# Performance work log

Hardware: AMD Instinct MI355X
Metric: run time of the kernel (lower is better)

Reference implementation:

```python
import jax, jax.numpy as jnp
import numpy as np

D_MODEL = 512
N_HEADS = 8
D_K = D_MODEL // N_HEADS  # 64
EPS = 1e-5


def setup_inputs() -> dict:
    key = jax.random.key(0)
    ks = jax.random.split(key, 16)
    s = 0.02
    B, T = 4, 2048
    return {
        "x": jax.random.normal(ks[0], (B, T, D_MODEL), dtype=jnp.float32),
        # per-head q/k/v projections stacked over heads: [H, d_model, d_k]
        "Wq": jax.random.normal(ks[1], (N_HEADS, D_MODEL, D_K), dtype=jnp.float32) * s,
        "bq": jnp.zeros((N_HEADS, D_K), dtype=jnp.float32),
        "Wk": jax.random.normal(ks[2], (N_HEADS, D_MODEL, D_K), dtype=jnp.float32) * s,
        "bk": jnp.zeros((N_HEADS, D_K), dtype=jnp.float32),
        "Wv": jax.random.normal(ks[3], (N_HEADS, D_MODEL, D_K), dtype=jnp.float32) * s,
        "bv": jnp.zeros((N_HEADS, D_K), dtype=jnp.float32),
        "Wp": jax.random.normal(ks[4], (D_MODEL, D_MODEL), dtype=jnp.float32) * s,
        "bp": jnp.zeros((D_MODEL,), dtype=jnp.float32),
        "W1": jax.random.normal(ks[5], (D_MODEL, 4 * D_MODEL), dtype=jnp.float32) * s,
        "b1": jnp.zeros((4 * D_MODEL,), dtype=jnp.float32),
        "W2": jax.random.normal(ks[6], (4 * D_MODEL, D_MODEL), dtype=jnp.float32) * s,
        "b2": jnp.zeros((D_MODEL,), dtype=jnp.float32),
        "g1": jnp.ones((D_MODEL,), dtype=jnp.float32),
        "be1": jnp.zeros((D_MODEL,), dtype=jnp.float32),
        "g2": jnp.ones((D_MODEL,), dtype=jnp.float32),
        "be2": jnp.zeros((D_MODEL,), dtype=jnp.float32),
    }


def _layer_norm(x, g, b):
    mu = jnp.mean(x, axis=-1, keepdims=True)
    var = jnp.var(x, axis=-1, keepdims=True)
    return (x - mu) * jax.lax.rsqrt(var + EPS) * g + b


def _block(x, Wq, bq, Wk, bk, Wv, bv, Wp, bp, W1, b1, W2, b2, g1, be1, g2, be2):
    B, T, _ = x.shape
    h = _layer_norm(x, g1, be1)
    # batched per-head projections: [B, H, T, d_k]
    q = jnp.einsum('btd,hdk->bhtk', h, Wq) + bq[:, None, :]
    k = jnp.einsum('btd,hdk->bhtk', h, Wk) + bk[:, None, :]
    v = jnp.einsum('btd,hdk->bhtk', h, Wv) + bv[:, None, :]
    scores = jnp.einsum('bhtk,bhsk->bhts', q, k)  # [B, H, T, T]
    causal = jnp.tril(jnp.ones((T, T), dtype=bool))
    # faithful to source: mask with -1e9 BEFORE dividing by sqrt(d_k)
    scores = jnp.where(causal, scores, jnp.float32(-1e9))
    attn = jax.nn.softmax(scores / jnp.float32(np.sqrt(D_K)), axis=-1)
    o = jnp.einsum('bhts,bhsk->bhtk', attn, v)  # [B, H, T, d_k]
    o = o.transpose(0, 2, 1, 3).reshape(B, T, D_MODEL)  # concat heads
    x = x + o @ Wp + bp
    h2 = _layer_norm(x, g2, be2)
    ff = jax.nn.relu(h2 @ W1 + b1) @ W2 + b2
    return x + ff


def reference(x, Wq, bq, Wk, bk, Wv, bv, Wp, bp, W1, b1, W2, b2, g1, be1, g2, be2):
    return _block(x, Wq, bq, Wk, bk, Wv, bv, Wp, bp, W1, b1, W2, b2, g1, be1, g2, be2)
```

## Files before the change

kernel.cpp:

```cpp
#include <hip/hip_runtime.h>
#include <hip/hip_bf16.h>
#include <math.h>

#define BATCH 4
#define SEQ   2048
#define DM    512
#define NH    8
#define DK    64
#define FF    2048
#define BT    (BATCH * SEQ)

#define SCALE_Q 0.18033688011112042f

typedef short bf16x8 __attribute__((ext_vector_type(8)));
typedef float f32x4  __attribute__((ext_vector_type(4)));

static __device__ inline short f2bf(float f) {
  union { float f; unsigned u; } v; v.f = f;
  unsigned r = (v.u + 0x7fffu + ((v.u >> 16) & 1u)) >> 16;
  return (short)r;
}

static __device__ __forceinline__ void gload16(const short* g, short* l) {
  __builtin_amdgcn_global_load_lds(
      (const __attribute__((address_space(1))) void*)g,
      (__attribute__((address_space(3))) void*)l, 16, 0, 0);
}

static __device__ __forceinline__ void xcd_swizzle(int& bx, int& by) {
  int gx = gridDim.x;
  int nwg = gx * gridDim.y;
  int id = blockIdx.x + gx * blockIdx.y;
  int nid = (id & 7) * (nwg >> 3) + (id >> 3);
  bx = nid % gx;
  by = nid / gx;
}

__global__ __launch_bounds__(256) void ln_kernel(
    const float* __restrict__ x, const float* __restrict__ gamma,
    const float* __restrict__ beta, short* __restrict__ out) {
  int row = blockIdx.x;
  const float* xr = x + (size_t)row * DM;
  int t = threadIdx.x;
  float v0 = xr[t], v1 = xr[t + 256];
  float s = v0 + v1;
  float sq = v0 * v0 + v1 * v1;
  for (int off = 32; off; off >>= 1) {
    s  += __shfl_xor(s, off);
    sq += __shfl_xor(sq, off);
  }
  __shared__ float ssum[4], ssq[4];
  int wave = t >> 6, lane = t & 63;
  if (lane == 0) { ssum[wave] = s; ssq[wave] = sq; }
  __syncthreads();
  if (t == 0) {
    float S = ssum[0] + ssum[1] + ssum[2] + ssum[3];
    float Q = ssq[0] + ssq[1] + ssq[2] + ssq[3];
    float mu = S * (1.0f / DM);
    float var = Q * (1.0f / DM) - mu * mu;
    ssum[0] = mu;
    ssq[0] = rsqrtf(var + 1e-5f);
  }
  __syncthreads();
  float mu = ssum[0], rstd = ssq[0];
  short* orow = out + (size_t)row * DM;
  orow[t]       = f2bf((v0 - mu) * rstd * gamma[t]       + beta[t]);
  orow[t + 256] = f2bf((v1 - mu) * rstd * gamma[t + 256] + beta[t + 256]);
}

__global__ __launch_bounds__(256) void wconv_kernel(
    const float* Wq, const float* Wk, const float* Wv,
    const float* Wp, const float* W1, const float* W2,
    short* wqkv, short* wpt, short* w1t, short* w2t) {
  int z = blockIdx.z;
  const float* src; short* dst; int R, C;
  if (z < 24) {
    int m = z >> 3, hh = z & 7;
    const float* s0 = (m == 0) ? Wq : (m == 1) ? Wk : Wv;
    src = s0 + (size_t)hh * 512 * 64;
    dst = wqkv + ((size_t)(m * 512 + hh * 64)) * 512;
    R = 512; C = 64;
  } else if (z == 24) { src = Wp; dst = wpt; R = 512;  C = 512;  }
  else if (z == 25)   { src = W1; dst = w1t; R = 512;  C = 2048; }
  else                { src = W2; dst = w2t; R = 2048; C = 512;  }
  int tx = blockIdx.x, ty = blockIdx.y;
  if (tx >= C / 64 || ty >= R / 64) return;
  __shared__ float Ts[64][68];
  int t = threadIdx.x;
  int r = t >> 2, c0 = (t & 3) * 16;
  const float* sp = src + (size_t)(ty * 64 + r) * C + tx * 64 + c0;
#pragma unroll
  for (int i = 0; i < 16; i += 4) {
    float4 v = *(const float4*)(sp + i);
    Ts[c0 + i + 0][r] = v.x; Ts[c0 + i + 1][r] = v.y;
    Ts[c0 + i + 2][r] = v.z; Ts[c0 + i + 3][r] = v.w;
  }
  __syncthreads();
  short* dp = dst + (size_t)(tx * 64 + r) * R + ty * 64 + c0;
  short tmp[16];
#pragma unroll
  for (int i = 0; i < 16; ++i) tmp[i] = f2bf(Ts[r][c0 + i]);
  *(int4*)(dp)     = *(int4*)&tmp[0];
  *(int4*)(dp + 8) = *(int4*)&tmp[8];
}

template<int TM, int TN>
__device__ __forceinline__ void gemm_core(
    const short* __restrict__ A, const short* __restrict__ Bw,
    int m0, int n0, int K, short* smem, f32x4 (&acc)[TM / 32][TN / 32]) {
  constexpr int AF = TM / 32, BF = TN / 32;
  constexpr int AC = TM / 64, BC = TN / 64;
  constexpr int BUFS = (TM + TN) * 32;
  int t = threadIdx.x;
  int wave = t >> 6, lane = t & 63, quad = lane >> 4, l16 = lane & 15;
  int wr = wave >> 1, wc = wave & 1;

  size_t aoff[AC], boff[BC];
  int aldsoff[AC], bldsoff[BC];
#pragma unroll
  for (int c = 0; c < AC; ++c) {
    int p = c * 256 + t, row = p >> 2, lg = (p & 3) ^ ((row >> 1) & 3);
    aoff[c] = (size_t)(m0 + row) * K + lg * 8;
    aldsoff[c] = c * 2048 + wave * 512;
  }
#pragma unroll
  for (int c = 0; c < BC; ++c) {
    int p = c * 256 + t, row = p >> 2, lg = (p & 3) ^ ((row >> 1) & 3);
    boff[c] = (size_t)(n0 + row) * K + lg * 8;
    bldsoff[c] = TM * 32 + c * 2048 + wave * 512;
  }

#pragma unroll
  for (int c = 0; c < AC; ++c) gload16(A + aoff[c], smem + aldsoff[c]);
#pragma unroll
  for (int c = 0; c < BC; ++c) gload16(Bw + boff[c], smem + bldsoff[c]);

  int physo = (quad ^ ((l16 >> 1) & 3)) * 8;

  for (int k0 = 0; k0 < K; k0 += 32) {
    short* cbuf = smem + ((k0 >> 5) & 1) * BUFS;
    __syncthreads();
    if (k0 + 32 < K) {
      short* nbuf = smem + (((k0 >> 5) & 1) ^ 1) * BUFS;
#pragma unroll
      for (int c = 0; c < AC; ++c) gload16(A + aoff[c] + k0 + 32, nbuf + aldsoff[c]);
#pragma unroll
      for (int c = 0; c < BC; ++c) gload16(Bw + boff[c] + k0 + 32, nbuf + bldsoff[c]);
    }
    bf16x8 af[AF], bfr[BF];
#pragma unroll
    for (int i = 0; i < AF; ++i)
      af[i] = *(const bf16x8*)&cbuf[(wr * (TM / 2) + i * 16 + l16) * 32 + physo];
#pragma unroll
    for (int j = 0; j < BF; ++j)
      bfr[j] = *(const bf16x8*)&cbuf[TM * 32 + (wc * (TN / 2) + j * 16 + l16) * 32 + physo];
#pragma unroll
    for (int i = 0; i < AF; ++i)
#pragma unroll
      for (int j = 0; j < BF; ++j)
        acc[i][j] = __builtin_amdgcn_mfma_f32_16x16x32_bf16(bfr[j], af[i], acc[i][j], 0, 0, 0);
  }
}

template<int TM, int TN>
__global__ __launch_bounds__(256) void mgemm_kernel(
    const short* __restrict__ A, const short* __restrict__ Bw,
    const float* __restrict__ bias, const float* __restrict__ res,
    void* __restrict__ C, int N, int K, int dorelu, int bf16out) {
  __shared__ __align__(16) short smem[(TM + TN) * 64];
  f32x4 acc[TM / 32][TN / 32];
  f32x4 zf = {0.f, 0.f, 0.f, 0.f};
#pragma unroll
  for (int i = 0; i < TM / 32; ++i)
#pragma unroll
    for (int j = 0; j < TN / 32; ++j) acc[i][j] = zf;
  int bx, by;
  xcd_swizzle(bx, by);
  int m0 = by * TM, n0 = bx * TN;
  gemm_core<TM, TN>(A, Bw, m0, n0, K, smem, acc);

  int t = threadIdx.x;
  int wave = t >> 6, lane = t & 63, quad = lane >> 4, l16 = lane & 15;
  int wr = wave >> 1, wc = wave & 1;
#pragma unroll
  for (int i = 0; i < TM / 32; ++i) {
    int m = m0 + wr * (TM / 2) + i * 16 + l16;
#pragma unroll
    for (int j = 0; j < TN / 32; ++j) {
      int nb = n0 + wc * (TN / 2) + j * 16 + quad * 4;
      float4 bv = *(const float4*)&bias[nb];
      float v[4] = {acc[i][j][0] + bv.x, acc[i][j][1] + bv.y,
                    acc[i][j][2] + bv.z, acc[i][j][3] + bv.w};
      if (dorelu) {
#pragma unroll
        for (int r = 0; r < 4; ++r) v[r] = fmaxf(v[r], 0.0f);
      }
      size_t off = (size_t)m * N + nb;
      if (res) {
        float4 rv = *(const float4*)(res + off);
        v[0] += rv.x; v[1] += rv.y; v[2] += rv.z; v[3] += rv.w;
      }
      if (bf16out) {
        short tmp[4] = {f2bf(v[0]), f2bf(v[1]), f2bf(v[2]), f2bf(v[3])};
        *(int2*)((short*)C + off) = *(int2*)tmp;
      } else {
        float4 outv = {v[0], v[1], v[2], v[3]};
        *(float4*)((float*)C + off) = outv;
      }
    }
  }
}

__global__ __launch_bounds__(256) void qkv_kernel(
    const short* __restrict__ A, const short* __restrict__ Bw,
    const float* __restrict__ bq, const float* __restrict__ bk,
    const float* __restrict__ bv,
    short* __restrict__ q, short* __restrict__ k, short* __restrict__ vt) {
  __shared__ __align__(16) short smem[17408];
  f32x4 acc[4][4];
  f32x4 zf = {0.f, 0.f, 0.f, 0.f};
#pragma unroll
  for (int i = 0; i < 4; ++i)
#pragma unroll
    for (int j = 0; j < 4; ++j) acc[i][j] = zf;
  int bx, by;
  xcd_swizzle(bx, by);
  int m0 = by * 128, n0 = bx * 128;
  gemm_core<128, 128>(A, Bw, m0, n0, DM, smem, acc);

  int t = threadIdx.x;
  int wave = t >> 6, lane = t & 63, quad = lane >> 4, l16 = lane & 15;
  int wr = wave >> 1, wc = wave & 1;

  if (n0 < 1024) {
    short* out = (n0 < 512) ? q : k;
    const float* bias = (n0 < 512) ? bq + n0 : bk + (n0 - 512);
    float scale = (n0 < 512) ? SCALE_Q : 1.0f;
    int ncol0 = (n0 < 512) ? n0 : n0 - 512;
#pragma unroll
    for (int i = 0; i < 4; ++i) {
      int m = m0 + wr * 64 + i * 16 + l16;
#pragma unroll
      for (int j = 0; j < 4; ++j) {
        int nb = wc * 64 + j * 16 + quad * 4;
        float4 bvv = *(const float4*)&bias[nb];
        short tmp[4];
        tmp[0] = f2bf((acc[i][j][0] + bvv.x) * scale);
        tmp[1] = f2bf((acc[i][j][1] + bvv.y) * scale);
        tmp[2] = f2bf((acc[i][j][2] + bvv.z) * scale);
        tmp[3] = f2bf((acc[i][j][3] + bvv.w) * scale);
        *(int2*)(out + (size_t)m * DM + ncol0 + nb) = *(int2*)tmp;
      }
    }
  } else {
    const float* bias = bv + (n0 - 1024);
    __syncthreads();
    short* Ts = smem;
#pragma unroll
    for (int i = 0; i < 4; ++i) {
      int ml = wr * 64 + i * 16 + l16;
#pragma unroll
      for (int j = 0; j < 4; ++j) {
        int nb = wc * 64 + j * 16 + quad * 4;
        float4 bvv = *(const float4*)&bias[nb];
        Ts[(nb + 0) * 136 + ml] = f2bf(acc[i][j][0] + bvv.x);
        Ts[(nb + 1) * 136 + ml] = f2bf(acc[i][j][1] + bvv.y);
        Ts[(nb + 2) * 136 + ml] = f2bf(acc[i][j][2] + bvv.z);
        Ts[(nb + 3) * 136 + ml] = f2bf(acc[i][j][3] + bvv.w);
      }
    }
    __syncthreads();
    int nl = t >> 1, half = (t & 1) * 64;
    int gn = (n0 - 1024) + nl;
    int hh = gn >> 6, dk = gn & 63;
    int bidx = m0 >> 11, s0 = (m0 & 2047) + half;
    short* dst = vt + ((size_t)((bidx * NH + hh) * DK + dk)) * SEQ + s0;
    const short* srcT = &Ts[nl * 136 + half];
#pragma unroll
    for (int i2 = 0; i2 < 64; i2 += 8)
      *(int4*)(dst + i2) = *(const int4*)(srcT + i2);
  }
}

template<bool DIAG>
static __device__ __forceinline__ void attn_tile(
    const short* __restrict__ KsC, const short* __restrict__ VsC,
    short* __restrict__ Psw, const bf16x8& qf0, const bf16x8& qf1,
    f32x4 (&o_acc)[4], float& l_part, int quad, int l16,
    int keyb0, int qrow) {
  f32x4 zf = {0.f, 0.f, 0.f, 0.f};
  int sw = l16 & 7;

#pragma unroll
  for (int nt = 0; nt < 4; ++nt) {
    int krow = nt * 16 + l16;
    bf16x8 ka0 = *(const bf16x8*)&KsC[krow * 64 + ((quad ^ sw) * 8)];
    bf16x8 ka1 = *(const bf16x8*)&KsC[krow * 64 + (((4 + quad) ^ sw) * 8)];
    f32x4 s = __builtin_amdgcn_mfma_f32_16x16x32_bf16(ka0, qf0, zf, 0, 0, 0);
    s = __builtin_amdgcn_mfma_f32_16x16x32_bf16(ka1, qf1, s, 0, 0, 0);
    int keyb = keyb0 + nt * 16 + quad * 4;
    float pr[4];
#pragma unroll
    for (int r = 0; r < 4; ++r) {
      float e = exp2f(s[r]);
      pr[r] = (DIAG && (keyb + r > qrow)) ? 0.0f : e;
      l_part += pr[r];
    }
    unsigned pk0 = __builtin_amdgcn_perm(
        __float_as_uint(pr[1]), __float_as_uint(pr[0]), 0x07060302u);
    unsigned pk1 = __builtin_amdgcn_perm(
        __float_as_uint(pr[3]), __float_as_uint(pr[2]), 0x07060302u);
    int2 w = {(int)pk0, (int)pk1};
    *(int2*)&Psw[l16 * 64 + (((nt * 2 + (quad >> 1)) ^ sw) << 3) +
                 ((quad & 1) * 4)] = w;
  }

  bf16x8 apf0 = *(const bf16x8*)&Psw[l16 * 64 + ((quad ^ sw) * 8)];
  bf16x8 apf1 = *(const bf16x8*)&Psw[l16 * 64 + (((4 + quad) ^ sw) * 8)];
  __builtin_amdgcn_s_setprio(1);
#pragma unroll
  for (int nt2 = 0; nt2 < 4; ++nt2) {
    int vrow = nt2 * 16 + l16;
    bf16x8 vf0 = *(const bf16x8*)&VsC[vrow * 64 + ((quad ^ sw) * 8)];
    bf16x8 vf1 = *(const bf16x8*)&VsC[vrow * 64 + (((4 + quad) ^ sw) * 8)];
    o_acc[nt2] = __builtin_amdgcn_mfma_f32_16x16x32_bf16(vf0, apf0, o_acc[nt2], 0, 0, 0);
    o_acc[nt2] = __builtin_amdgcn_mfma_f32_16x16x32_bf16(vf1, apf1, o_acc[nt2], 0, 0, 0);
  }
  __builtin_amdgcn_s_setprio(0);
}

__global__ __launch_bounds__(256) void fattn_kernel(
    const short* __restrict__ Q, const short* __restrict__ Kg,
    const short* __restrict__ Vt, short* __restrict__ O) {
  int id = blockIdx.x + 32 * (blockIdx.y + NH * blockIdx.z);
  int c = id & 7, j = id >> 3;
  int g = c * 4 + (j & 3);
  int qt = 31 - (j >> 2);
  int h = g & 7, b = g >> 3;
  int q0 = qt * 64;
  int t = threadIdx.x, wave = t >> 6, lane = t & 63, quad = lane >> 4, l16 = lane & 15;

  __shared__ __align__(16) short Ks[2][64 * 64];
  __shared__ __align__(16) short Vs[2][64 * 64];
  __shared__ __align__(16) short Ps[4][16 * 64];

  f32x4 zf = {0.f, 0.f, 0.f, 0.f};
  const short* qp = Q + ((size_t)(b * SEQ + q0 + wave * 16 + l16)) * DM + h * DK;
  bf16x8 qf0 = *(const bf16x8*)(qp + quad * 8);
  bf16x8 qf1 = *(const bf16x8*)(qp + 32 + quad * 8);

  f32x4 o_acc[4];
  float l_part = 0.0f;
#pragma unroll
  for (int i = 0; i < 4; ++i) o_acc[i] = zf;

  const short* kb = Kg + ((size_t)(b * SEQ)) * DM + h * DK;
  const short* vb = Vt + ((size_t)((b * NH + h) * DK)) * SEQ;

  int row0 = t >> 3,         lg0 = (t & 7) ^ (row0 & 7);
  int row1 = (256 + t) >> 3, lg1 = ((256 + t) & 7) ^ (row1 & 7);
  const short* kp0 = kb + (size_t)row0 * DM + lg0 * 8;
  const short* kp1 = kb + (size_t)row1 * DM + lg1 * 8;
  const short* vp0 = vb + (size_t)row0 * SEQ + lg0 * 8;
  const short* vp1 = vb + (size_t)row1 * SEQ + lg1 * 8;
  int lo0 = wave * 512, lo1 = 2048 + wave * 512;

#define STAGE_KV(B) do {                                     \
    gload16(kp0, &Ks[B][lo0]); gload16(kp1, &Ks[B][lo1]);    \
    gload16(vp0, &Vs[B][lo0]); gload16(vp1, &Vs[B][lo1]);    \
    kp0 += 64 * DM; kp1 += 64 * DM; vp0 += 64; vp1 += 64; } while (0)

  STAGE_KV(0);

  int qrow = q0 + wave * 16 + l16;
  short* Psw = &Ps[wave][0];

  int buf = 0;
  for (int kt = 0; kt < qt; ++kt) {
    __syncthreads();
    STAGE_KV(buf ^ 1);
    attn_tile<false>(&Ks[buf][0], &Vs[buf][0], Psw, qf0, qf1,
                     o_acc, l_part, quad, l16, 0, qrow);
    buf ^= 1;
  }
  __syncthreads();
  attn_tile<true>(&Ks[buf][0], &Vs[buf][0], Psw, qf0, qf1,
                  o_acc, l_part, quad, l16, qt * 64, qrow);

  float lf = l_part;
  lf += __shfl_xor(lf, 16);
  lf += __shfl_xor(lf, 32);
  float inv = 1.0f / lf;
  short* orow = O + ((size_t)(b * SEQ) + qrow) * DM + h * DK;
#pragma unroll
  for (int nt2 = 0; nt2 < 4; ++nt2) {
    short tmp[4];
#pragma unroll
    for (int r = 0; r < 4; ++r) tmp[r] = f2bf(o_acc[nt2][r] * inv);
    *(int2*)(orow + nt2 * 16 + quad * 4) = *(int2*)tmp;
  }
#undef STAGE_KV
}

extern "C" void kernel_launch(void* const* d_in, const int* in_sizes, int n_in,
                              void* d_out, int out_size, void* d_ws, size_t ws_size,
                              hipStream_t stream) {
  const float* x   = (const float*)d_in[0];
  const float* Wq  = (const float*)d_in[1];
  const float* bq  = (const float*)d_in[2];
  const float* Wk  = (const float*)d_in[3];
  const float* bk  = (const float*)d_in[4];
  const float* Wv  = (const float*)d_in[5];
  const float* bv  = (const float*)d_in[6];
  const float* Wp  = (const float*)d_in[7];
  const float* bp  = (const float*)d_in[8];
  const float* W1  = (const float*)d_in[9];
  const float* b1  = (const float*)d_in[10];
  const float* W2  = (const float*)d_in[11];
  const float* b2  = (const float*)d_in[12];
  const float* g1  = (const float*)d_in[13];
  const float* be1 = (const float*)d_in[14];
  const float* g2  = (const float*)d_in[15];
  const float* be2 = (const float*)d_in[16];
  float* out = (float*)d_out;

  char* wsb = (char*)d_ws;
  const size_t SB = (size_t)BT * DM * 2;
  short* h    = (short*)(wsb);
  short* q    = (short*)(wsb + SB);
  short* k    = (short*)(wsb + 2 * SB);
  short* vt   = (short*)(wsb + 3 * SB);
  short* o    = (short*)(wsb + 4 * SB);
  float* x2   = (float*)(wsb + 5 * SB);
  short* h2   = (short*)(wsb + 5 * SB + (size_t)BT * DM * 4);
  short* ff   = (short*)(wsb + 6 * SB + (size_t)BT * DM * 4);
  short* wqkv = (short*)(wsb + 6 * SB + (size_t)BT * DM * 4 + (size_t)BT * FF * 2);
  short* wpt  = wqkv + 1536 * 512;
  short* w1t  = wpt + 512 * 512;
  short* w2t  = w1t + 2048 * 512;

  dim3 blk(256);

  wconv_kernel<<<dim3(32, 32, 27), blk, 0, stream>>>(Wq, Wk, Wv, Wp, W1, W2,
                                                     wqkv, wpt, w1t, w2t);
  ln_kernel<<<BT, blk, 0, stream>>>(x, g1, be1, h);

  qkv_kernel<<<dim3(12, 64), blk, 0, stream>>>(h, wqkv, bq, bk, bv, q, k, vt);

  fattn_kernel<<<dim3(32, NH, BATCH), blk, 0, stream>>>(q, k, vt, o);

  mgemm_kernel<128, 64><<<dim3(8, 64), blk, 0, stream>>>(o, wpt, bp, x, x2, DM, DM, 0, 0);
  ln_kernel<<<BT, blk, 0, stream>>>(x2, g2, be2, h2);
  mgemm_kernel<128, 128><<<dim3(16, 64), blk, 0, stream>>>(h2, w1t, b1, nullptr, ff, FF, DM, 1, 1);
  mgemm_kernel<128, 64><<<dim3(8, 64), blk, 0, stream>>>(ff, w2t, b2, x2, out, DM, FF, 0, 0);
}
```

Before: 273.4 us.

## Add 64x64-tile GEMM for N=512 projections and compact weight-conversion grid

Adds a dedicated 64x64 tiled bf16 MFMA GEMM kernel with double-buffered LDS loads and uses it for the output projection and the FFN down-projection. Launching 1024 blocks instead of 512 should fill the GPU's CUs better on these N=512 GEMMs. The trade-off is more per-tile load overhead and less reuse. Separately, the weight-conversion launch drops from a 32x32x27 grid, where most blocks exit immediately, to a flat 768-block grid with no idle blocks.

```diff
diff --git a/kernel.cpp b/kernel.cpp
--- a/kernel.cpp
+++ b/kernel.cpp
@@ -72,19 +72,25 @@
     const float* Wq, const float* Wk, const float* Wv,
     const float* Wp, const float* W1, const float* W2,
     short* wqkv, short* wpt, short* w1t, short* w2t) {
-  int z = blockIdx.z;
-  const float* src; short* dst; int R, C;
-  if (z < 24) {
+  int id = blockIdx.x;
+  const float* src; short* dst; int R, C, tx, ty;
+  if (id < 192) {
+    int z = id >> 3;
     int m = z >> 3, hh = z & 7;
     const float* s0 = (m == 0) ? Wq : (m == 1) ? Wk : Wv;
     src = s0 + (size_t)hh * 512 * 64;
     dst = wqkv + ((size_t)(m * 512 + hh * 64)) * 512;
-    R = 512; C = 64;
-  } else if (z == 24) { src = Wp; dst = wpt; R = 512;  C = 512;  }
-  else if (z == 25)   { src = W1; dst = w1t; R = 512;  C = 2048; }
-  else                { src = W2; dst = w2t; R = 2048; C = 512;  }
-  int tx = blockIdx.x, ty = blockIdx.y;
-  if (tx >= C / 64 || ty >= R / 64) return;
+    R = 512; C = 64; tx = 0; ty = id & 7;
+  } else if (id < 256) {
+    int w = id - 192; src = Wp; dst = wpt; R = 512; C = 512;
+    tx = w & 7; ty = w >> 3;
+  } else if (id < 512) {
+    int w = id - 256; src = W1; dst = w1t; R = 512; C = 2048;
+    tx = w & 31; ty = w >> 5;
+  } else {
+    int w = id - 512; src = W2; dst = w2t; R = 2048; C = 512;
+    tx = w & 7; ty = w >> 3;
+  }
   __shared__ float Ts[64][68];
   int t = threadIdx.x;
   int r = t >> 2, c0 = (t & 3) * 16;
@@ -188,6 +194,101 @@
 #pragma unroll
     for (int j = 0; j < TN / 32; ++j) {
       int nb = n0 + wc * (TN / 2) + j * 16 + quad * 4;
+      float4 bv = *(const float4*)&bias[nb];
+      float v[4] = {acc[i][j][0] + bv.x, acc[i][j][1] + bv.y,
+                    acc[i][j][2] + bv.z, acc[i][j][3] + bv.w};
+      if (dorelu) {
+#pragma unroll
+        for (int r = 0; r < 4; ++r) v[r] = fmaxf(v[r], 0.0f);
+      }
+      size_t off = (size_t)m * N + nb;
+      if (res) {
+        float4 rv = *(const float4*)(res + off);
+        v[0] += rv.x; v[1] += rv.y; v[2] += rv.z; v[3] += rv.w;
+      }
+      if (bf16out) {
+        short tmp[4] = {f2bf(v[0]), f2bf(v[1]), f2bf(v[2]), f2bf(v[3])};
+        *(int2*)((short*)C + off) = *(int2*)tmp;
+      } else {
+        float4 outv = {v[0], v[1], v[2], v[3]};
+        *(float4*)((float*)C + off) = outv;
+      }
+    }
+  }
+}
+
+__global__ __launch_bounds__(256) void mgemm64_kernel(
+    const short* __restrict__ A, const short* __restrict__ Bw,
+    const float* __restrict__ bias, const float* __restrict__ res,
+    void* __restrict__ C, int N, int K, int dorelu, int bf16out) {
+  __shared__ __align__(16) short smem[2 * 8192];
+  f32x4 acc[2][2];
+  f32x4 zf = {0.f, 0.f, 0.f, 0.f};
+#pragma unroll
+  for (int i = 0; i < 2; ++i)
+#pragma unroll
+    for (int j = 0; j < 2; ++j) acc[i][j] = zf;
+  int bx, by;
+  xcd_swizzle(bx, by);
+  int m0 = by * 64, n0 = bx * 64;
+
+  int t = threadIdx.x;
+  int wave = t >> 6, lane = t & 63, quad = lane >> 4, l16 = lane & 15;
+  int wr = wave >> 1, wc = wave & 1;
+
+  int rA0 = t >> 3,        lg0 = (t & 7) ^ (rA0 & 7);
+  int rA1 = 32 + (t >> 3), lg1 = (t & 7) ^ (rA1 & 7);
+  size_t aoff0 = (size_t)(m0 + rA0) * K + lg0 * 8;
+  size_t aoff1 = (size_t)(m0 + rA1) * K + lg1 * 8;
+  size_t boff0 = (size_t)(n0 + rA0) * K + lg0 * 8;
+  size_t boff1 = (size_t)(n0 + rA1) * K + lg1 * 8;
+  int lo0 = wave * 512, lo1 = 2048 + wave * 512;
+
+  gload16(A + aoff0, smem + lo0);
+  gload16(A + aoff1, smem + lo1);
+  gload16(Bw + boff0, smem + 4096 + lo0);
+  gload16(Bw + boff1, smem + 4096 + lo1);
+
+  int sw = l16 & 7;
+
+  for (int k0 = 0; k0 < K; k0 += 64) {
+    short* cbuf = smem + ((k0 >> 6) & 1) * 8192;
+    __syncthreads();
+    if (k0 + 64 < K) {
+      short* nbuf = smem + (((k0 >> 6) & 1) ^ 1) * 8192;
+      gload16(A + aoff0 + k0 + 64, nbuf + lo0);
+      gload16(A + aoff1 + k0 + 64, nbuf + lo1);
+      gload16(Bw + boff0 + k0 + 64, nbuf + 4096 + lo0);
+      gload16(Bw + boff1 + k0 + 64, nbuf + 4096 + lo1);
+    }
+    bf16x8 af0[2], af1[2], bf0[2], bf1[2];
+#pragma unroll
+    for (int i = 0; i < 2; ++i) {
+      int r = wr * 32 + i * 16 + l16;
+      af0[i] = *(const bf16x8*)&cbuf[r * 64 + ((quad ^ sw) * 8)];
+      af1[i] = *(const bf16x8*)&cbuf[r * 64 + (((4 + quad) ^ sw) * 8)];
+    }
+#pragma unroll
+    for (int j = 0; j < 2; ++j) {
+      int r = wc * 32 + j * 16 + l16;
+      bf0[j] = *(const bf16x8*)&cbuf[4096 + r * 64 + ((quad ^ sw) * 8)];
+      bf1[j] = *(const bf16x8*)&cbuf[4096 + r * 64 + (((4 + quad) ^ sw) * 8)];
+    }
+#pragma unroll
+    for (int i = 0; i < 2; ++i)
+#pragma unroll
+      for (int j = 0; j < 2; ++j) {
+        acc[i][j] = __builtin_amdgcn_mfma_f32_16x16x32_bf16(bf0[j], af0[i], acc[i][j], 0, 0, 0);
+        acc[i][j] = __builtin_amdgcn_mfma_f32_16x16x32_bf16(bf1[j], af1[i], acc[i][j], 0, 0, 0);
+      }
+  }
+
+#pragma unroll
+  for (int i = 0; i < 2; ++i) {
+    int m = m0 + wr * 32 + i * 16 + l16;
+#pragma unroll
+    for (int j = 0; j < 2; ++j) {
+      int nb = n0 + wc * 32 + j * 16 + quad * 4;
       float4 bv = *(const float4*)&bias[nb];
       float v[4] = {acc[i][j][0] + bv.x, acc[i][j][1] + bv.y,
                     acc[i][j][2] + bv.z, acc[i][j][3] + bv.w};
@@ -441,16 +542,16 @@
 
   dim3 blk(256);
 
-  wconv_kernel<<<dim3(32, 32, 27), blk, 0, stream>>>(Wq, Wk, Wv, Wp, W1, W2,
-                                                     wqkv, wpt, w1t, w2t);
+  wconv_kernel<<<dim3(768), blk, 0, stream>>>(Wq, Wk, Wv, Wp, W1, W2,
+                                              wqkv, wpt, w1t, w2t);
   ln_kernel<<<BT, blk, 0, stream>>>(x, g1, be1, h);
 
   qkv_kernel<<<dim3(12, 64), blk, 0, stream>>>(h, wqkv, bq, bk, bv, q, k, vt);
 
   fattn_kernel<<<dim3(32, NH, BATCH), blk, 0, stream>>>(q, k, vt, o);
 
-  mgemm_kernel<128, 64><<<dim3(8, 64), blk, 0, stream>>>(o, wpt, bp, x, x2, DM, DM, 0, 0);
+  mgemm64_kernel<<<dim3(8, 128), blk, 0, stream>>>(o, wpt, bp, x, x2, DM, DM, 0, 0);
   ln_kernel<<<BT, blk, 0, stream>>>(x2, g2, be2, h2);
   mgemm_kernel<128, 128><<<dim3(16, 64), blk, 0, stream>>>(h2, w1t, b1, nullptr, ff, FF, DM, 1, 1);
-  mgemm_kernel<128, 64><<<dim3(8, 64), blk, 0, stream>>>(ff, w2t, b2, x2, out, DM, FF, 0, 0);
-}
+  mgemm64_kernel<<<dim3(8, 128), blk, 0, stream>>>(ff, w2t, b2, x2, out, DM, FF, 0, 0);
+}
```

After: 255.7 us. -6.4%, faster.
